# Optimization experiments

Hardware: AMD Instinct MI355X
Metric: run time of the kernel (lower is better)

Reference implementation:

```python
import jax, jax.numpy as jnp
import numpy as np

N, E, B = 32768, 524288, 256
IN_N, IN_E, HID, L = 6, 2, 64, 3
STATE_DIM, ACT_DIM = 16, 2
MLP1, MLP2 = 256, 256
EPS_AGG, EPS_BN = 1e-6, 1e-5


def setup_inputs() -> dict:
    key = jax.random.key(0)
    ks = iter(jax.random.split(key, 48))
    def nrm(shape, scale=0.05):
        return jax.random.normal(next(ks), shape, dtype=jnp.float32) * scale
    inp = {
        'h': jax.random.normal(next(ks), (N, IN_N), dtype=jnp.float32),
        # edge features are inverted (1/e) in the model, so keep them positive
        'e_feat': jax.random.uniform(next(ks), (E, IN_E), dtype=jnp.float32, minval=0.5, maxval=1.5),
        'src': jax.random.randint(next(ks), (E,), 0, N, dtype=jnp.int32),
        'dst': jax.random.randint(next(ks), (E,), 0, N, dtype=jnp.int32),
        'graph_ids': jnp.sort(jax.random.randint(next(ks), (N,), 0, B, dtype=jnp.int32)),
        'state': jax.random.normal(next(ks), (B, STATE_DIM), dtype=jnp.float32),
        'action': jax.random.normal(next(ks), (B, ACT_DIM), dtype=jnp.float32),
        'emb_h_W': nrm((IN_N, HID)), 'emb_h_b': jnp.zeros((HID,), jnp.float32),
        'emb_e_W': nrm((IN_E, HID)), 'emb_e_b': jnp.zeros((HID,), jnp.float32),
        'A_W': nrm((L, HID, HID)), 'A_b': jnp.zeros((L, HID), jnp.float32),
        'B_W': nrm((L, HID, HID)), 'B_b': jnp.zeros((L, HID), jnp.float32),
        'C_W': nrm((L, HID, HID)), 'C_b': jnp.zeros((L, HID), jnp.float32),
        'D_W': nrm((L, HID, HID)), 'D_b': jnp.zeros((L, HID), jnp.float32),
        'E_W': nrm((L, HID, HID)), 'E_b': jnp.zeros((L, HID), jnp.float32),
        'bn_h_g': jnp.ones((L, HID), jnp.float32), 'bn_h_beta': jnp.zeros((L, HID), jnp.float32),
        'bn_e_g': jnp.ones((L, HID), jnp.float32), 'bn_e_beta': jnp.zeros((L, HID), jnp.float32),
        'l1_W': nrm((HID + STATE_DIM + ACT_DIM, MLP1)), 'l1_b': jnp.zeros((MLP1,), jnp.float32),
        'l2_W': nrm((MLP1, MLP2)), 'l2_b': jnp.zeros((MLP2,), jnp.float32),
        'l3_W': nrm((MLP2, 1)), 'l3_b': jnp.zeros((1,), jnp.float32),
    }
    return inp


def _batch_norm(x, g, b):
    # BatchNorm1d in training mode: normalize over the node/edge axis
    mu = jnp.mean(x, axis=0)
    var = jnp.var(x, axis=0)
    return g * (x - mu) * jax.lax.rsqrt(var + EPS_BN) + b


def _forward(h, e_feat, src, dst, graph_ids, state, action,
             emb_h_W, emb_h_b, emb_e_W, emb_e_b,
             A_W, A_b, B_W, B_b, C_W, C_b, D_W, D_b, E_W, E_b,
             bn_h_g, bn_h_beta, bn_e_g, bn_e_beta,
             l1_W, l1_b, l2_W, l2_b, l3_W, l3_b):
    e = 1.0 / e_feat                       # model feeds reciprocal edge features
    h = h @ emb_h_W + emb_h_b              # [N, HID]
    e = e @ emb_e_W + emb_e_b              # [E, HID]
    n = h.shape[0]
    for l in range(L):
        Ah = h @ A_W[l] + A_b[l]
        Bh = h @ B_W[l] + B_b[l]
        Dh = h @ D_W[l] + D_b[l]
        Eh = h @ E_W[l] + E_b[l]
        Ce = e @ C_W[l] + C_b[l]
        e_hat = Ce + Dh[src] + Eh[dst]     # edge update [E, HID]
        sigma = jax.nn.sigmoid(e_hat)
        num = jax.ops.segment_sum(sigma * Bh[src], dst, num_segments=n)
        den = jax.ops.segment_sum(sigma, dst, num_segments=n)
        h_new = Ah + num / (den + EPS_AGG)
        h = h + jax.nn.relu(_batch_norm(h_new, bn_h_g[l], bn_h_beta[l]))  # residual
        e = e + jax.nn.relu(_batch_norm(e_hat, bn_e_g[l], bn_e_beta[l]))
    # mean readout per graph
    counts = jax.ops.segment_sum(jnp.ones((n,), h.dtype), graph_ids, num_segments=B)
    hg = jax.ops.segment_sum(h, graph_ids, num_segments=B) / jnp.maximum(counts, 1.0)[:, None]
    x = jnp.concatenate([hg, state, action], axis=-1)
    x = jax.nn.relu(x @ l1_W + l1_b)
    x = jax.nn.relu(x @ l2_W + l2_b)
    return x @ l3_W + l3_b                 # [B, 1]


def reference(h, e_feat, src, dst, graph_ids, state, action,
              emb_h_W, emb_h_b, emb_e_W, emb_e_b,
              A_W, A_b, B_W, B_b, C_W, C_b, D_W, D_b, E_W, E_b,
              bn_h_g, bn_h_beta, bn_e_g, bn_e_beta,
              l1_W, l1_b, l2_W, l2_b, l3_W, l3_b):
    return _forward(h, e_feat, src, dst, graph_ids, state, action,
                    emb_h_W, emb_h_b, emb_e_W, emb_e_b,
                    A_W, A_b, B_W, B_b, C_W, C_b, D_W, D_b, E_W, E_b,
                    bn_h_g, bn_h_beta, bn_e_g, bn_e_beta,
                    l1_W, l1_b, l2_W, l2_b, l3_W, l3_b)
```

## Files before the change

kernel.cpp:

```cpp
#include <hip/hip_runtime.h>
#include <math.h>

#define NN 32768
#define NE 524288
#define NB 256
#define HID 64
#define NL 3
#define EPS_AGG 1e-6f
#define EPS_BN 1e-5f
#define AGG_BLOCKS 512
#define EF_BLOCKS 1024
#define NG_BLOCKS 128

typedef _Float16 h16;
typedef h16 h16x8 __attribute__((ext_vector_type(8)));
typedef h16 h16x4 __attribute__((ext_vector_type(4)));
typedef float f32x4 __attribute__((ext_vector_type(4)));

#define MFMA16(a, b, c) __builtin_amdgcn_mfma_f32_16x16x32_f16(a, b, c, 0, 0, 0)


__global__ void k_zero4(float4* __restrict__ p, long n4) {
    long t = (long)blockIdx.x * blockDim.x + threadIdx.x;
    long stride = (long)gridDim.x * blockDim.x;
    float4 z = {0.f, 0.f, 0.f, 0.f};
    for (; t < n4; t += stride) p[t] = z;
}

__global__ void k_zero_stats(float* __restrict__ s) { s[threadIdx.x] = 0.f; }


__global__ void k_hist(const int* __restrict__ dst, int* __restrict__ hist) {
    int i = blockIdx.x * blockDim.x + threadIdx.x;
    atomicAdd(&hist[dst[i]], 1);
}

__global__ void k_scan(const int* __restrict__ hist, int* __restrict__ rowptr,
                       int* __restrict__ cursor) {
    __shared__ int part[1024];
    int t = threadIdx.x;
    int loc[32];
    int base = t * 32, sum = 0;
#pragma unroll
    for (int k = 0; k < 32; ++k) { loc[k] = hist[base + k]; sum += loc[k]; }
    part[t] = sum;
    __syncthreads();
    for (int off = 1; off < 1024; off <<= 1) {
        int v = (t >= off) ? part[t - off] : 0;
        __syncthreads();
        part[t] += v;
        __syncthreads();
    }
    int ex = part[t] - sum;
#pragma unroll
    for (int k = 0; k < 32; ++k) {
        rowptr[base + k] = ex; cursor[base + k] = ex; ex += loc[k];
    }
    if (t == 1023) rowptr[NN] = ex;
}

__global__ void k_scatter(const int* __restrict__ src, const int* __restrict__ dst,
                          int* __restrict__ cursor, int* __restrict__ eperm,
                          int* __restrict__ src_s, int* __restrict__ dst_s) {
    int i = blockIdx.x * blockDim.x + threadIdx.x;
    int d = dst[i];
    int pos = atomicAdd(&cursor[d], 1);
    eperm[pos] = i;
    src_s[pos] = src[i];
    dst_s[pos] = d;
}


__global__ void k_ghist(const int* __restrict__ gid, int* __restrict__ ghist) {
    int i = blockIdx.x * blockDim.x + threadIdx.x;
    atomicAdd(&ghist[gid[i]], 1);
}

__global__ void k_gscan(const int* __restrict__ ghist, int* __restrict__ grp) {
    __shared__ int part[256];
    int t = threadIdx.x;
    int v = ghist[t];
    part[t] = v;
    __syncthreads();
    for (int off = 1; off < 256; off <<= 1) {
        int u = (t >= off) ? part[t - off] : 0;
        __syncthreads();
        part[t] += u;
        __syncthreads();
    }
    grp[t + 1] = part[t];
    if (t == 0) grp[0] = 0;
}


__global__ void k_embed_h(const float* __restrict__ hin, const float* __restrict__ W,
                          const float* __restrict__ b, float* __restrict__ out,
                          h16* __restrict__ out16) {
    int tid = blockIdx.x * blockDim.x + threadIdx.x;
    int i = tid >> 6, j = tid & 63;
    float acc = b[j];
#pragma unroll
    for (int k = 0; k < 6; ++k) acc += hin[i * 6 + k] * W[k * 64 + j];
    out[tid] = acc;
    out16[tid] = (h16)acc;
}

__global__ void k_embed_e_perm(const float* __restrict__ ef, const int* __restrict__ eperm,
                               const float* __restrict__ W, const float* __restrict__ b,
                               h16* __restrict__ out) {
    int t = blockIdx.x * blockDim.x + threadIdx.x;
    int pos = t >> 3, j0 = (t & 7) * 8;
    int i = eperm[pos];
    float r0 = 1.0f / ef[i * 2 + 0];
    float r1 = 1.0f / ef[i * 2 + 1];
    float4 b0 = *(const float4*)&b[j0],      b1 = *(const float4*)&b[j0 + 4];
    float4 w00 = *(const float4*)&W[j0],     w01 = *(const float4*)&W[j0 + 4];
    float4 w10 = *(const float4*)&W[64 + j0], w11 = *(const float4*)&W[64 + j0 + 4];
    h16x8 o;
    o[0] = (h16)(b0.x + r0 * w00.x + r1 * w10.x);
    o[1] = (h16)(b0.y + r0 * w00.y + r1 * w10.y);
    o[2] = (h16)(b0.z + r0 * w00.z + r1 * w10.z);
    o[3] = (h16)(b0.w + r0 * w00.w + r1 * w10.w);
    o[4] = (h16)(b1.x + r0 * w01.x + r1 * w11.x);
    o[5] = (h16)(b1.y + r0 * w01.y + r1 * w11.y);
    o[6] = (h16)(b1.z + r0 * w01.z + r1 * w11.z);
    o[7] = (h16)(b1.w + r0 * w01.w + r1 * w11.w);
    *(h16x8*)&out[(size_t)pos * 64 + j0] = o;
}


__global__ void k_node_gemm4(const h16* __restrict__ X,
                             const float* __restrict__ AW, const float* __restrict__ Ab,
                             const float* __restrict__ BW, const float* __restrict__ Bb,
                             const float* __restrict__ DW, const float* __restrict__ Db,
                             const float* __restrict__ EW, const float* __restrict__ Eb,
                             float* __restrict__ Ah, h16* __restrict__ Bh,
                             h16* __restrict__ Dh, h16* __restrict__ Eh) {
    __shared__ h16 w[4][4096];
    __shared__ float tr[4][16][68];
    const float* Ws[4] = {AW, BW, DW, EW};
#pragma unroll
    for (int m = 0; m < 4; ++m)
        for (int i = threadIdx.x; i < 4096; i += 256) {
            int c = i >> 6, k = i & 63;
            w[m][i] = (h16)Ws[m][k * 64 + c];
        }
    __syncthreads();
    int lane = threadIdx.x & 63, wid = threadIdx.x >> 6;
    int ar = lane & 15, ak = (lane >> 4) * 8;
    int r = lane >> 2, c0 = (lane & 3) * 16;
    float bias[4][4];
    const float* Bs[4] = {Ab, Bb, Db, Eb};
#pragma unroll
    for (int m = 0; m < 4; ++m)
#pragma unroll
        for (int ct = 0; ct < 4; ++ct) bias[m][ct] = Bs[m][ct * 16 + ar];
    for (int tile = blockIdx.x * 4 + wid; tile < NN / 16; tile += NG_BLOCKS * 4) {
        int row0 = tile * 16;
        h16x8 a0 = *(const h16x8*)&X[(size_t)(row0 + ar) * 64 + ak];
        h16x8 a1 = *(const h16x8*)&X[(size_t)(row0 + ar) * 64 + 32 + ak];
#pragma unroll
        for (int m = 0; m < 4; ++m) {
#pragma unroll
            for (int ct = 0; ct < 4; ++ct) {
                int col = ct * 16 + ar;
                float bv = bias[m][ct];
                f32x4 acc = (f32x4){bv, bv, bv, bv};
                h16x8 b0 = *(const h16x8*)&w[m][col * 64 + ak];
                h16x8 b1 = *(const h16x8*)&w[m][col * 64 + 32 + ak];
                acc = MFMA16(a0, b0, acc);
                acc = MFMA16(a1, b1, acc);
#pragma unroll
                for (int j = 0; j < 4; ++j)
                    tr[wid][(lane >> 4) * 4 + j][ct * 16 + ar] = acc[j];
            }
            if (m == 0) {
#pragma unroll
                for (int j = 0; j < 4; ++j)
                    *(float4*)&Ah[(size_t)(row0 + r) * 64 + c0 + j * 4] =
                        *(float4*)&tr[wid][r][c0 + j * 4];
            } else {
                h16* out = (m == 1) ? Bh : (m == 2) ? Dh : Eh;
                h16x8 o0, o1;
#pragma unroll
                for (int j = 0; j < 8; ++j) {
                    o0[j] = (h16)tr[wid][r][c0 + j];
                    o1[j] = (h16)tr[wid][r][c0 + 8 + j];
                }
                *(h16x8*)&out[(size_t)(row0 + r) * 64 + c0] = o0;
                *(h16x8*)&out[(size_t)(row0 + r) * 64 + c0 + 8] = o1;
            }
        }
    }
}


template <int MODE>
__global__ void k_edge_fwd(const h16* __restrict__ e, h16* __restrict__ ewr,
                           const float* __restrict__ CW, const float* __restrict__ Cb,
                           const h16* __restrict__ Dh, const h16* __restrict__ Eh,
                           const int* __restrict__ src_s, const int* __restrict__ dst_s,
                           h16* __restrict__ ehat, const float* __restrict__ stats) {
    __shared__ h16 w[4096];
    __shared__ float tr[4][16][68];
    for (int i = threadIdx.x; i < 4096; i += 256) {
        int c = i >> 6, k = i & 63;
        w[i] = (h16)CW[k * 64 + c];
    }
    __syncthreads();
    int lane = threadIdx.x & 63, wid = threadIdx.x >> 6;
    int ar = lane & 15, ak = (lane >> 4) * 8;
    int r = lane >> 2, c0 = (lane & 3) * 16;
    h16x8 wb0[4], wb1[4];
    float bias[4];
#pragma unroll
    for (int ct = 0; ct < 4; ++ct) {
        int col = ct * 16 + ar;
        wb0[ct] = *(const h16x8*)&w[col * 64 + ak];
        wb1[ct] = *(const h16x8*)&w[col * 64 + 32 + ak];
        bias[ct] = Cb[col];
    }
    float sc0[8], sh0[8], sc1[8], sh1[8];
    if (MODE != 0) {
#pragma unroll
        for (int k = 0; k < 8; ++k) {
            sc0[k] = stats[256 + ak + k];      sh0[k] = stats[320 + ak + k];
            sc1[k] = stats[256 + 32 + ak + k]; sh1[k] = stats[320 + 32 + ak + k];
        }
    }
    for (int tile = blockIdx.x * 4 + wid; tile < NE / 16; tile += EF_BLOCKS * 4) {
        int e0 = tile * 16;
        size_t fbase = (size_t)(e0 + ar) * 64;
        h16x8 a0, a1;
        if (MODE == 0) {
            a0 = *(const h16x8*)&e[fbase + ak];
            a1 = *(const h16x8*)&e[fbase + 32 + ak];
        } else {
            h16x8 ep0 = *(const h16x8*)&e[fbase + ak];
            h16x8 ep1 = *(const h16x8*)&e[fbase + 32 + ak];
            h16x8 eh0 = *(const h16x8*)&ehat[fbase + ak];
            h16x8 eh1 = *(const h16x8*)&ehat[fbase + 32 + ak];
#pragma unroll
            for (int k = 0; k < 8; ++k) {
                a0[k] = (h16)((float)ep0[k] + fmaxf(0.f, (float)eh0[k] * sc0[k] + sh0[k]));
                a1[k] = (h16)((float)ep1[k] + fmaxf(0.f, (float)eh1[k] * sc1[k] + sh1[k]));
            }
            if (MODE == 1) {
                *(h16x8*)&ewr[fbase + ak] = a0;
                *(h16x8*)&ewr[fbase + 32 + ak] = a1;
            }
        }
        int er = e0 + r;
        int s = src_s[er], d = dst_s[er];
#pragma unroll
        for (int ct = 0; ct < 4; ++ct) {
            float bv = bias[ct];
            f32x4 acc = (f32x4){bv, bv, bv, bv};
            acc = MFMA16(a0, wb0[ct], acc);
            acc = MFMA16(a1, wb1[ct], acc);
#pragma unroll
            for (int j = 0; j < 4; ++j)
                tr[wid][(lane >> 4) * 4 + j][ct * 16 + ar] = acc[j];
        }
        h16x8 d0 = *(const h16x8*)&Dh[(size_t)s * 64 + c0];
        h16x8 d1 = *(const h16x8*)&Dh[(size_t)s * 64 + c0 + 8];
        h16x8 g0 = *(const h16x8*)&Eh[(size_t)d * 64 + c0];
        h16x8 g1 = *(const h16x8*)&Eh[(size_t)d * 64 + c0 + 8];
        h16x8 o0, o1;
#pragma unroll
        for (int j = 0; j < 8; ++j) {
            o0[j] = (h16)(tr[wid][r][c0 + j] + (float)d0[j] + (float)g0[j]);
            o1[j] = (h16)(tr[wid][r][c0 + 8 + j] + (float)d1[j] + (float)g1[j]);
        }
        *(h16x8*)&ehat[(size_t)er * 64 + c0] = o0;
        *(h16x8*)&ehat[(size_t)er * 64 + c0 + 8] = o1;
    }
}


__global__ void k_agg_node(const h16* __restrict__ ehat, const h16* __restrict__ Bh,
                           const int* __restrict__ src_s, const int* __restrict__ rowptr,
                           const float* __restrict__ Ah, float* __restrict__ hnew,
                           float* __restrict__ stats) {
    __shared__ float red[256];
    int lane = threadIdx.x & 63, wid = threadIdx.x >> 6;
    int wglob = blockIdx.x * 4 + wid;
    float esum = 0.f, esq = 0.f, hsum = 0.f, hsq = 0.f;
    for (int d = wglob; d < NN; d += AGG_BLOCKS * 4) {
        int begin = rowptr[d], end = rowptr[d + 1];
        float accn = 0.f, accd = 0.f;
        int p = begin;
        for (; p + 8 <= end; p += 8) {
            int   ss[8]; float eh[8], bh[8];
#pragma unroll
            for (int q = 0; q < 8; ++q) ss[q] = src_s[p + q];
#pragma unroll
            for (int q = 0; q < 8; ++q) eh[q] = (float)ehat[(size_t)(p + q) * 64 + lane];
#pragma unroll
            for (int q = 0; q < 8; ++q) bh[q] = (float)Bh[(size_t)ss[q] * 64 + lane];
#pragma unroll
            for (int q = 0; q < 8; ++q) {
                float ev = eh[q];
                esum += ev; esq += ev * ev;
                float sg = 1.0f / (1.0f + __expf(-ev));
                accn += sg * bh[q]; accd += sg;
            }
        }
        if (p + 4 <= end) {
            int   ss[4]; float eh[4], bh[4];
#pragma unroll
            for (int q = 0; q < 4; ++q) ss[q] = src_s[p + q];
#pragma unroll
            for (int q = 0; q < 4; ++q) eh[q] = (float)ehat[(size_t)(p + q) * 64 + lane];
#pragma unroll
            for (int q = 0; q < 4; ++q) bh[q] = (float)Bh[(size_t)ss[q] * 64 + lane];
#pragma unroll
            for (int q = 0; q < 4; ++q) {
                float ev = eh[q];
                esum += ev; esq += ev * ev;
                float sg = 1.0f / (1.0f + __expf(-ev));
                accn += sg * bh[q]; accd += sg;
            }
            p += 4;
        }
        for (; p < end; ++p) {
            float ev = (float)ehat[(size_t)p * 64 + lane];
            int s = src_s[p];
            float bv = (float)Bh[(size_t)s * 64 + lane];
            esum += ev; esq += ev * ev;
            float sg = 1.0f / (1.0f + __expf(-ev));
            accn += sg * bv; accd += sg;
        }
        float hv = Ah[(size_t)d * 64 + lane] + accn / (accd + EPS_AGG);
        hnew[(size_t)d * 64 + lane] = hv;
        hsum += hv; hsq += hv * hv;
    }
    float vals[4] = {esum, esq, hsum, hsq};
#pragma unroll
    for (int s2 = 0; s2 < 4; ++s2) {
        red[wid * 64 + lane] = vals[s2];
        __syncthreads();
        if (wid == 0)
            atomicAdd(&stats[s2 * 64 + lane],
                      red[lane] + red[64 + lane] + red[128 + lane] + red[192 + lane]);
        __syncthreads();
    }
}


__global__ void k_finstats2(float* __restrict__ stats, const float* __restrict__ eg,
                            const float* __restrict__ eb, const float* __restrict__ hgm,
                            const float* __restrict__ hbt) {
    int t = threadIdx.x;
    float o1, o2; int i1, i2;
    if (t < 64) {
        float mu = stats[t] / (float)NE;
        float var = stats[64 + t] / (float)NE - mu * mu;
        float rs = rsqrtf(var + EPS_BN);
        float g = eg[t];
        o1 = g * rs; o2 = eb[t] - g * mu * rs;
        i1 = 256 + t; i2 = 320 + t;
    } else {
        int j = t - 64;
        float mu = stats[128 + j] / (float)NN;
        float var = stats[192 + j] / (float)NN - mu * mu;
        float rs = rsqrtf(var + EPS_BN);
        float g = hgm[j];
        o1 = g * rs; o2 = hbt[j] - g * mu * rs;
        i1 = 384 + j; i2 = 448 + j;
    }
    __syncthreads();
    stats[t] = 0.f; stats[128 + t] = 0.f;
    stats[i1] = o1; stats[i2] = o2;
}


__global__ void k_hbn_apply(float* __restrict__ h, h16* __restrict__ h16buf,
                            const float* __restrict__ hnew,
                            const float* __restrict__ stats) {
    int t = blockIdx.x * blockDim.x + threadIdx.x;
    int j4 = t & 15;
    float4 s = ((const float4*)(stats + 384))[j4];
    float4 b = ((const float4*)(stats + 448))[j4];
    float4 v = ((const float4*)hnew)[t];
    float4 x = ((const float4*)h)[t];
    x.x += fmaxf(0.f, v.x * s.x + b.x);
    x.y += fmaxf(0.f, v.y * s.y + b.y);
    x.z += fmaxf(0.f, v.z * s.z + b.z);
    x.w += fmaxf(0.f, v.w * s.w + b.w);
    ((float4*)h)[t] = x;
    h16x4 o;
    o[0] = (h16)x.x; o[1] = (h16)x.y; o[2] = (h16)x.z; o[3] = (h16)x.w;
    *(h16x4*)&h16buf[(size_t)t * 4] = o;
}


__global__ void k_graph_mean(const float* __restrict__ h, const int* __restrict__ grp,
                             float* __restrict__ hg) {
    int lane = threadIdx.x & 63, wid = threadIdx.x >> 6;
    int g = blockIdx.x * 4 + wid;
    int begin = grp[g], end = grp[g + 1];
    float acc = 0.f;
    int i = begin;
    for (; i + 4 <= end; i += 4) {
        float a0 = h[(size_t)(i + 0) * 64 + lane];
        float a1 = h[(size_t)(i + 1) * 64 + lane];
        float a2 = h[(size_t)(i + 2) * 64 + lane];
        float a3 = h[(size_t)(i + 3) * 64 + lane];
        acc += (a0 + a1) + (a2 + a3);
    }
    for (; i < end; ++i) acc += h[(size_t)i * 64 + lane];
    float cnt = (float)(end - begin);
    hg[g * 64 + lane] = acc / fmaxf(cnt, 1.0f);
}


__global__ void k_mlp1(const float* __restrict__ hg, const float* __restrict__ st,
                       const float* __restrict__ ac, const float* __restrict__ W,
                       const float* __restrict__ b, float* __restrict__ out) {
    __shared__ float x[82];
    int bidx = blockIdx.x, t = threadIdx.x;
    if (t < 64) x[t] = hg[bidx * 64 + t];
    else if (t < 80) x[t] = st[bidx * 16 + (t - 64)];
    else if (t < 82) x[t] = ac[bidx * 2 + (t - 80)];
    __syncthreads();
    float acc = b[t];
#pragma unroll
    for (int k = 0; k < 82; ++k) acc += x[k] * W[k * 256 + t];
    out[bidx * 256 + t] = fmaxf(acc, 0.f);
}

__global__ void k_mlp2(const float* __restrict__ xin, const float* __restrict__ W,
                       const float* __restrict__ b, float* __restrict__ out) {
    __shared__ float x[256];
    int bidx = blockIdx.x, t = threadIdx.x;
    x[t] = xin[bidx * 256 + t];
    __syncthreads();
    float acc = b[t];
#pragma unroll 8
    for (int k = 0; k < 256; ++k) acc += x[k] * W[k * 256 + t];
    out[bidx * 256 + t] = fmaxf(acc, 0.f);
}

__global__ void k_mlp3(const float* __restrict__ xin, const float* __restrict__ W,
                       const float* __restrict__ b, float* __restrict__ out) {
    int t = threadIdx.x;
    float acc = b[0];
#pragma unroll 8
    for (int k = 0; k < 256; ++k) acc += xin[t * 256 + k] * W[k];
    out[t] = acc;
}


extern "C" void kernel_launch(void* const* d_in, const int* in_sizes, int n_in,
                              void* d_out, int out_size, void* d_ws, size_t ws_size,
                              hipStream_t stream) {
    const float* in_h   = (const float*)d_in[0];
    const float* e_feat = (const float*)d_in[1];
    const int*   src    = (const int*)d_in[2];
    const int*   dst    = (const int*)d_in[3];
    const int*   gid    = (const int*)d_in[4];
    const float* state  = (const float*)d_in[5];
    const float* action = (const float*)d_in[6];
    const float* embhW  = (const float*)d_in[7];
    const float* embhb  = (const float*)d_in[8];
    const float* embeW  = (const float*)d_in[9];
    const float* embeb  = (const float*)d_in[10];
    const float* A_W = (const float*)d_in[11]; const float* A_b = (const float*)d_in[12];
    const float* B_W = (const float*)d_in[13]; const float* B_b = (const float*)d_in[14];
    const float* C_W = (const float*)d_in[15]; const float* C_b = (const float*)d_in[16];
    const float* D_W = (const float*)d_in[17]; const float* D_b = (const float*)d_in[18];
    const float* E_W = (const float*)d_in[19]; const float* E_b = (const float*)d_in[20];
    const float* bnhg = (const float*)d_in[21]; const float* bnhb = (const float*)d_in[22];
    const float* bneg = (const float*)d_in[23]; const float* bneb = (const float*)d_in[24];
    const float* l1W = (const float*)d_in[25]; const float* l1b = (const float*)d_in[26];
    const float* l2W = (const float*)d_in[27]; const float* l2b = (const float*)d_in[28];
    const float* l3W = (const float*)d_in[29]; const float* l3b = (const float*)d_in[30];

    char* base = (char*)d_ws;
    size_t off = 0;
    auto alloc = [&](size_t bytes) {
        off = (off + 255) & ~(size_t)255;
        void* p = base + off; off += bytes; return p;
    };
    h16*   e_s    = (h16*)  alloc((size_t)NE * 64 * 2);
    h16*   ehat   = (h16*)  alloc((size_t)NE * 64 * 2);
    float* h      = (float*)alloc((size_t)NN * 64 * 4);
    h16*   h16buf = (h16*)  alloc((size_t)NN * 64 * 2);
    float* Ah     = (float*)alloc((size_t)NN * 64 * 4);
    float* hnew   = (float*)alloc((size_t)NN * 64 * 4);
    h16*   Bh     = (h16*)  alloc((size_t)NN * 64 * 2);
    h16*   Dh     = (h16*)  alloc((size_t)NN * 64 * 2);
    h16*   Eh     = (h16*)  alloc((size_t)NN * 64 * 2);
    float* stats  = (float*)alloc(512 * 4);
    float* hg     = (float*)alloc((size_t)NB * 64 * 4);
    float* x1     = (float*)alloc((size_t)NB * 256 * 4);
    float* x2     = (float*)alloc((size_t)NB * 256 * 4);
    int*   eperm  = (int*)  alloc((size_t)NE * 4);
    int*   src_s  = (int*)  alloc((size_t)NE * 4);
    int*   dst_s  = (int*)  alloc((size_t)NE * 4);
    int*   hist   = (int*)  alloc((size_t)NN * 4);
    int*   ghist  = (int*)  alloc(256 * 4);
    int*   rowptr = (int*)  alloc((size_t)(NN + 1) * 4);
    int*   cursor = (int*)  alloc((size_t)NN * 4);
    int*   grp    = (int*)  alloc((size_t)(NB + 1) * 4);
    size_t need = off;

    if (ws_size < need) return;

    k_zero4<<<33, 256, 0, stream>>>((float4*)hist, ((long)NN * 4 + 256 * 4) / 16);
    k_hist<<<NE / 256, 256, 0, stream>>>(dst, hist);
    k_scan<<<1, 1024, 0, stream>>>(hist, rowptr, cursor);
    k_scatter<<<NE / 256, 256, 0, stream>>>(src, dst, cursor, eperm, src_s, dst_s);
    k_ghist<<<NN / 256, 256, 0, stream>>>(gid, ghist);
    k_gscan<<<1, 256, 0, stream>>>(ghist, grp);

    k_embed_h<<<(NN * 64) / 256, 256, 0, stream>>>(in_h, embhW, embhb, h, h16buf);
    k_embed_e_perm<<<(NE * 8) / 256, 256, 0, stream>>>(e_feat, eperm, embeW, embeb, e_s);

    k_zero_stats<<<1, 256, 0, stream>>>(stats);
    for (int l = 0; l < NL; ++l) {
        k_node_gemm4<<<NG_BLOCKS, 256, 0, stream>>>(h16buf,
                                                    A_W + l * 4096, A_b + l * 64,
                                                    B_W + l * 4096, B_b + l * 64,
                                                    D_W + l * 4096, D_b + l * 64,
                                                    E_W + l * 4096, E_b + l * 64,
                                                    Ah, Bh, Dh, Eh);
        if (l == 0)
            k_edge_fwd<0><<<EF_BLOCKS, 256, 0, stream>>>(e_s, nullptr,
                C_W + l * 4096, C_b + l * 64, Dh, Eh, src_s, dst_s, ehat, stats);
        else if (l == 1)
            k_edge_fwd<1><<<EF_BLOCKS, 256, 0, stream>>>(e_s, e_s,
                C_W + l * 4096, C_b + l * 64, Dh, Eh, src_s, dst_s, ehat, stats);
        else
            k_edge_fwd<2><<<EF_BLOCKS, 256, 0, stream>>>(e_s, nullptr,
                C_W + l * 4096, C_b + l * 64, Dh, Eh, src_s, dst_s, ehat, stats);
        k_agg_node<<<AGG_BLOCKS, 256, 0, stream>>>(ehat, Bh, src_s, rowptr, Ah, hnew, stats);
        k_finstats2<<<1, 128, 0, stream>>>(stats, bneg + l * 64, bneb + l * 64,
                                           bnhg + l * 64, bnhb + l * 64);
        k_hbn_apply<<<NN / 16, 256, 0, stream>>>(h, h16buf, hnew, stats);
    }

    k_graph_mean<<<NB / 4, 256, 0, stream>>>(h, grp, hg);

    k_mlp1<<<NB, 256, 0, stream>>>(hg, state, action, l1W, l1b, x1);
    k_mlp2<<<NB, 256, 0, stream>>>(x1, l2W, l2b, x2);
    k_mlp3<<<1, NB, 0, stream>>>(x2, l3W, l3b, (float*)d_out);
}
```

Measured before the change: 613.5 us.

## Raise grid sizes and spread BN stat atomics across banked accumulators

Increases the block counts for the aggregation, edge and node-GEMM kernels so more work is in flight on the GPU. With four times as many aggregation blocks, the batch-norm statistics atomics are spread over 16 banks indexed by block ID, and the finalize kernel sums the banks and clears them. This is meant to reduce atomic contention on a single 256-float stats array. In exchange the finalize kernel does more reads and zeroing, and the larger grids add launch and per-block overhead.

```diff
diff --git a/kernel.cpp b/kernel.cpp
--- a/kernel.cpp
+++ b/kernel.cpp
@@ -8,9 +8,14 @@
 #define NL 3
 #define EPS_AGG 1e-6f
 #define EPS_BN 1e-5f
-#define AGG_BLOCKS 512
-#define EF_BLOCKS 1024
-#define NG_BLOCKS 128
+#define AGG_BLOCKS 2048
+#define EF_BLOCKS 2048
+#define NG_BLOCKS 512
+#define NBANK 16
+#define S_ESC 4096
+#define S_ESH 4160
+#define S_HSC 4224
+#define S_HSH 4288
 
 typedef _Float16 h16;
 typedef h16 h16x8 __attribute__((ext_vector_type(8)));
@@ -26,8 +31,6 @@
     float4 z = {0.f, 0.f, 0.f, 0.f};
     for (; t < n4; t += stride) p[t] = z;
 }
-
-__global__ void k_zero_stats(float* __restrict__ s) { s[threadIdx.x] = 0.f; }
 
 
 __global__ void k_hist(const int* __restrict__ dst, int* __restrict__ hist) {
@@ -224,8 +227,8 @@
     if (MODE != 0) {
 #pragma unroll
         for (int k = 0; k < 8; ++k) {
-            sc0[k] = stats[256 + ak + k];      sh0[k] = stats[320 + ak + k];
-            sc1[k] = stats[256 + 32 + ak + k]; sh1[k] = stats[320 + 32 + ak + k];
+            sc0[k] = stats[S_ESC + ak + k];      sh0[k] = stats[S_ESH + ak + k];
+            sc1[k] = stats[S_ESC + 32 + ak + k]; sh1[k] = stats[S_ESH + 32 + ak + k];
         }
     }
     for (int tile = blockIdx.x * 4 + wid; tile < NE / 16; tile += EF_BLOCKS * 4) {
@@ -336,12 +339,13 @@
         hsum += hv; hsq += hv * hv;
     }
     float vals[4] = {esum, esq, hsum, hsq};
+    int bank = blockIdx.x & (NBANK - 1);
 #pragma unroll
     for (int s2 = 0; s2 < 4; ++s2) {
         red[wid * 64 + lane] = vals[s2];
         __syncthreads();
         if (wid == 0)
-            atomicAdd(&stats[s2 * 64 + lane],
+            atomicAdd(&stats[bank * 256 + s2 * 64 + lane],
                       red[lane] + red[64 + lane] + red[128 + lane] + red[192 + lane]);
         __syncthreads();
     }
@@ -352,25 +356,40 @@
                             const float* __restrict__ eb, const float* __restrict__ hgm,
                             const float* __restrict__ hbt) {
     int t = threadIdx.x;
+    float s1 = 0.f, s2 = 0.f;
+    if (t < 64) {
+#pragma unroll
+        for (int b = 0; b < NBANK; ++b) {
+            s1 += stats[b * 256 + t];
+            s2 += stats[b * 256 + 64 + t];
+        }
+    } else {
+        int j = t - 64;
+#pragma unroll
+        for (int b = 0; b < NBANK; ++b) {
+            s1 += stats[b * 256 + 128 + j];
+            s2 += stats[b * 256 + 192 + j];
+        }
+    }
     float o1, o2; int i1, i2;
     if (t < 64) {
-        float mu = stats[t] / (float)NE;
-        float var = stats[64 + t] / (float)NE - mu * mu;
+        float mu = s1 / (float)NE;
+        float var = s2 / (float)NE - mu * mu;
         float rs = rsqrtf(var + EPS_BN);
         float g = eg[t];
         o1 = g * rs; o2 = eb[t] - g * mu * rs;
-        i1 = 256 + t; i2 = 320 + t;
+        i1 = S_ESC + t; i2 = S_ESH + t;
     } else {
         int j = t - 64;
-        float mu = stats[128 + j] / (float)NN;
-        float var = stats[192 + j] / (float)NN - mu * mu;
+        float mu = s1 / (float)NN;
+        float var = s2 / (float)NN - mu * mu;
         float rs = rsqrtf(var + EPS_BN);
         float g = hgm[j];
         o1 = g * rs; o2 = hbt[j] - g * mu * rs;
-        i1 = 384 + j; i2 = 448 + j;
-    }
-    __syncthreads();
-    stats[t] = 0.f; stats[128 + t] = 0.f;
+        i1 = S_HSC + j; i2 = S_HSH + j;
+    }
+    __syncthreads();
+    for (int i = t; i < NBANK * 256; i += 128) stats[i] = 0.f;
     stats[i1] = o1; stats[i2] = o2;
 }
 
@@ -380,8 +399,8 @@
                             const float* __restrict__ stats) {
     int t = blockIdx.x * blockDim.x + threadIdx.x;
     int j4 = t & 15;
-    float4 s = ((const float4*)(stats + 384))[j4];
-    float4 b = ((const float4*)(stats + 448))[j4];
+    float4 s = ((const float4*)(stats + S_HSC))[j4];
+    float4 b = ((const float4*)(stats + S_HSH))[j4];
     float4 v = ((const float4*)hnew)[t];
     float4 x = ((const float4*)h)[t];
     x.x += fmaxf(0.f, v.x * s.x + b.x);
@@ -492,7 +511,7 @@
     h16*   Bh     = (h16*)  alloc((size_t)NN * 64 * 2);
     h16*   Dh     = (h16*)  alloc((size_t)NN * 64 * 2);
     h16*   Eh     = (h16*)  alloc((size_t)NN * 64 * 2);
-    float* stats  = (float*)alloc(512 * 4);
+    float* stats  = (float*)alloc((NBANK * 256 + 512) * 4);
     float* hg     = (float*)alloc((size_t)NB * 64 * 4);
     float* x1     = (float*)alloc((size_t)NB * 256 * 4);
     float* x2     = (float*)alloc((size_t)NB * 256 * 4);
@@ -518,7 +537,7 @@
     k_embed_h<<<(NN * 64) / 256, 256, 0, stream>>>(in_h, embhW, embhb, h, h16buf);
     k_embed_e_perm<<<(NE * 8) / 256, 256, 0, stream>>>(e_feat, eperm, embeW, embeb, e_s);
 
-    k_zero_stats<<<1, 256, 0, stream>>>(stats);
+    k_zero4<<<4, 256, 0, stream>>>((float4*)stats, (NBANK * 256) / 4);
     for (int l = 0; l < NL; ++l) {
         k_node_gemm4<<<NG_BLOCKS, 256, 0, stream>>>(h16buf,
                                                     A_W + l * 4096, A_b + l * 64,
```

Result: faster. 568.5 us (-7.3%).
